# Kernel optimization log

Hardware: AMD Instinct MI355X
Metric: run time of the kernel (lower is better)

Reference implementation:

```python
import jax, jax.numpy as jnp
import numpy as np
import math

DIM = 1024
N_HEADS = 16
HEAD_DIM = DIM // N_HEADS


def rope(x):
    # x: [B, H, S, D] with D == HEAD_DIM, interleaved even/odd rotation
    S = x.shape[-2]
    D = x.shape[-1]
    pos = jnp.arange(S, dtype=x.dtype)[:, None]              # [S, 1]
    dim = jnp.arange(D // 2, dtype=x.dtype)[None, :]         # [1, D/2]
    theta = pos / jnp.exp(2.0 * dim / D * math.log(10000.0))  # [S, D/2]
    sin = jnp.sin(theta)[None, None]                          # [1,1,S,D/2]
    cos = jnp.cos(theta)[None, None]
    x1 = x[..., ::2]
    x2 = x[..., 1::2]
    out1 = x1 * cos - x2 * sin
    out2 = x1 * sin + x2 * cos
    # interleave back: stack on last axis then flatten pairs
    return jnp.stack([out1, out2], axis=-1).reshape(x.shape)


def setup_inputs() -> dict:
    key = jax.random.key(0)
    ks = jax.random.split(key, 9)
    B, S = 2, 2048
    s = 1.0 / math.sqrt(DIM)
    inp = {
        "x": jax.random.normal(ks[0], (B, S, DIM), dtype=jnp.float32),
        "wq": jax.random.normal(ks[1], (DIM, DIM), dtype=jnp.float32) * s,
        "bq": jnp.zeros((DIM,), dtype=jnp.float32),
        "wk": jax.random.normal(ks[2], (DIM, DIM), dtype=jnp.float32) * s,
        "bk": jnp.zeros((DIM,), dtype=jnp.float32),
        "wv": jax.random.normal(ks[3], (DIM, DIM), dtype=jnp.float32) * s,
        "bv": jnp.zeros((DIM,), dtype=jnp.float32),
        "wo": jax.random.normal(ks[4], (DIM, DIM), dtype=jnp.float32) * s,
        "bo": jnp.zeros((DIM,), dtype=jnp.float32),
    }
    return inp


def reference(x, wq, bq, wk, bk, wv, bv, wo, bo):
    B, S, _ = x.shape
    # torch Linear: y = x @ W^T + b
    def proj(w, b):
        y = jnp.einsum('bsd,ed->bse', x, w) + b
        return y.reshape(B, S, N_HEADS, HEAD_DIM).transpose(0, 2, 1, 3)  # [B,H,S,Dh]
    q = rope(proj(wq, bq))
    k = rope(proj(wk, bk))
    v = proj(wv, bv)
    score = jnp.einsum('bhqd,bhkd->bhqk', q, k) / math.sqrt(HEAD_DIM)
    causal = jnp.tril(jnp.ones((S, S), dtype=bool))
    score = jnp.where(causal[None, None], score, -jnp.inf)
    attn = jax.nn.softmax(score, axis=-1)
    out = jnp.einsum('bhqk,bhkd->bhqd', attn, v)
    out = out.transpose(0, 2, 1, 3).reshape(B, S, DIM)
    return jnp.einsum('bsd,ed->bse', out, wo) + bo
```

## Files before the change

### kernel.cpp

```cpp
#include <hip/hip_runtime.h>
#include <cstdint>
#include <cstddef>
#include <cmath>


typedef __bf16 bf16_t;
typedef __bf16 bf16x8 __attribute__((ext_vector_type(8)));
typedef __bf16 bf16x4 __attribute__((ext_vector_type(4)));
typedef float  f32x4  __attribute__((ext_vector_type(4)));

#define DEVFN __device__ __forceinline__

static constexpr int Bn  = 2;
static constexpr int S   = 2048;
static constexpr int DIM = 1024;
static constexpr int NH  = 16;
static constexpr int HD  = 64;
static constexpr int Mrows = Bn * S;

DEVFN f32x4 mfma16(bf16x8 a, bf16x8 b, f32x4 c) {
  return __builtin_amdgcn_mfma_f32_16x16x32_bf16(a, b, c, 0, 0, 0);
}

DEVFN void gl_lds16(const bf16_t* g, bf16_t* l) {
  __builtin_amdgcn_global_load_lds(
      (const __attribute__((address_space(1))) unsigned*)g,
      (__attribute__((address_space(3))) unsigned*)l, 16, 0, 0);
}

DEVFN float fast_exp2(float x) { return exp2f(x); }

__global__ __launch_bounds__(256) void k_prep(
    const float* __restrict__ x, const float* __restrict__ wq,
    const float* __restrict__ wk, const float* __restrict__ wv,
    const float* __restrict__ wo, bf16_t* __restrict__ xb,
    bf16_t* __restrict__ wqb, bf16_t* __restrict__ wkb,
    bf16_t* __restrict__ wvb, bf16_t* __restrict__ wob,
    float2* __restrict__ tab) {
  const int bid = blockIdx.x;
  if (bid < 8192) {
    const float* src;
    bf16_t* dst;
    size_t base;
    if (bid < 4096) {
      src = x; dst = xb; base = (size_t)bid << 10;
    } else {
      int wsel = (bid - 4096) >> 10;
      src = wsel == 0 ? wq : wsel == 1 ? wk : wsel == 2 ? wv : wo;
      dst = wsel == 0 ? wqb : wsel == 1 ? wkb : wsel == 2 ? wvb : wob;
      base = (size_t)((bid - 4096) & 1023) << 10;
    }
    size_t i = base + (size_t)threadIdx.x * 4;
    float4 v = *(const float4*)(src + i);
    bf16x4 o = { (bf16_t)v.x, (bf16_t)v.y, (bf16_t)v.z, (bf16_t)v.w };
    *(bf16x4*)(dst + i) = o;
  } else {
    int i = (bid - 8192) * 256 + threadIdx.x;
    int s = i >> 5, d = i & 31;
    float th = (float)s * expf((float)d * -0.2878231366f);
    tab[i] = make_float2(cosf(th), sinf(th));
  }
}

__global__ __launch_bounds__(256) void k_gemm_qkv(
    const bf16_t* __restrict__ A, const bf16_t* __restrict__ Wall,
    const float* __restrict__ c0, const float* __restrict__ c1,
    const float* __restrict__ c2, bf16_t* __restrict__ Oq,
    bf16_t* __restrict__ Ok, bf16_t* __restrict__ VTo,
    const float2* __restrict__ tab) {
  __shared__ __align__(16) bf16_t Al[128 * 64];
  __shared__ __align__(16) bf16_t Bl[64 * 64];
  const int t = threadIdx.x, w = t >> 6, l = t & 63;
  const int lr = l & 15, lc = l >> 4;
  const int lid = blockIdx.x;
  const int xcd = lid & 7, s = lid >> 3;
  const int my = ((xcd >> 1) << 3) + (s & 7);
  const int nx = (xcd & 1) * 24 + (s >> 3);
  const int m0 = my * 128, n0g = nx * 64;
  const int z = n0g >> 10, n0l = n0g & 1023;
  f32x4 acc[2][4] = {};

  for (int k0 = 0; k0 < DIM; k0 += 64) {
    __syncthreads();
#pragma unroll
    for (int ld = 0; ld < 4; ++ld) {
      int c = t + ld * 256;
      int row = c >> 3;
      int j = ((c & 7) ^ (row & 7)) << 3;
      gl_lds16(A + (size_t)(m0 + row) * DIM + k0 + j,
               Al + (size_t)(w * 64 + ld * 256) * 8);
    }
#pragma unroll
    for (int ld = 0; ld < 2; ++ld) {
      int c = t + ld * 256;
      int row = c >> 3;
      int j = ((c & 7) ^ (row & 7)) << 3;
      gl_lds16(Wall + (size_t)(n0g + row) * DIM + k0 + j,
               Bl + (size_t)(w * 64 + ld * 256) * 8);
    }
    asm volatile("s_waitcnt vmcnt(0)" ::: "memory");
    __syncthreads();
    bf16x8 af[2][2], bfr[2][4];
#pragma unroll
    for (int ks = 0; ks < 2; ++ks) {
#pragma unroll
      for (int mi = 0; mi < 2; ++mi) {
        int row = w * 32 + mi * 16 + lr;
        int off = ((ks * 4 + lc) << 4) ^ ((row & 7) << 4);
        af[ks][mi] = *(const bf16x8*)((const char*)Al + row * 128 + off);
      }
#pragma unroll
      for (int ni = 0; ni < 4; ++ni) {
        int row = ni * 16 + lr;
        int off = ((ks * 4 + lc) << 4) ^ ((row & 7) << 4);
        bfr[ks][ni] = *(const bf16x8*)((const char*)Bl + row * 128 + off);
      }
    }
    __builtin_amdgcn_s_setprio(1);
#pragma unroll
    for (int ks = 0; ks < 2; ++ks)
#pragma unroll
      for (int mi = 0; mi < 2; ++mi)
#pragma unroll
        for (int ni = 0; ni < 4; ++ni)
          acc[mi][ni] = mfma16(af[ks][mi], bfr[ks][ni], acc[mi][ni]);
    __builtin_amdgcn_s_setprio(0);
  }

  if (z == 2) {
    const int h = n0l >> 6;
#pragma unroll
    for (int ni = 0; ni < 4; ++ni) {
      const int d = ni * 16 + lr;
      const float bv = c2[n0l + ni * 16 + lr];
#pragma unroll
      for (int mi = 0; mi < 2; ++mi) {
        int rowb = m0 + w * 32 + mi * 16 + lc * 4;
        int bb = rowb >> 11, ss = rowb & (S - 1);
        bf16x4 pb = { (bf16_t)(acc[mi][ni][0] + bv),
                      (bf16_t)(acc[mi][ni][1] + bv),
                      (bf16_t)(acc[mi][ni][2] + bv),
                      (bf16_t)(acc[mi][ni][3] + bv) };
        *(bf16x4*)(VTo + ((size_t)(bb * NH + h) * HD + d) * S + ss) = pb;
      }
    }
  } else {
    bf16_t* Ov = z == 0 ? Oq : Ok;
    const float* bias = z == 0 ? c0 : c1;
    const float scale = z == 0 ? 0.125f * 1.4426950408889634f : 1.0f;
#pragma unroll
    for (int ni = 0; ni < 4; ++ni) {
      const int col = n0l + ni * 16 + lr;
      const float bv = bias[col];
      const int p0 = ni * 8 + (lr >> 1);
#pragma unroll
      for (int mi = 0; mi < 2; ++mi) {
#pragma unroll
        for (int r = 0; r < 4; ++r) {
          int row = m0 + w * 32 + mi * 16 + lc * 4 + r;
          float v = acc[mi][ni][r] + bv;
          float pt = __shfl_xor(v, 1);
          float2 cs = tab[(row & (S - 1)) * 32 + p0];
          float out = (lr & 1) ? (pt * cs.y + v * cs.x)
                               : (v * cs.x - pt * cs.y);
          Ov[(size_t)row * DIM + col] = (bf16_t)(out * scale);
        }
      }
    }
  }
}

__global__ __launch_bounds__(256) void k_gemm_out(
    const bf16_t* __restrict__ A, const bf16_t* __restrict__ Bw,
    const float* __restrict__ bias, float* __restrict__ Ov) {
  __shared__ __align__(16) bf16_t Al[64 * 64];
  __shared__ __align__(16) bf16_t Bl[64 * 64];
  const int t = threadIdx.x, w = t >> 6, l = t & 63;
  const int lr = l & 15, lc = l >> 4;
  const int lid = blockIdx.x;
  const int xcd = lid & 7, s = lid >> 3;
  const int my = ((xcd >> 1) << 4) + (s & 15);
  const int nx = (xcd & 1) * 8 + (s >> 4);
  const int m0 = my * 64, n0 = nx * 64;
  f32x4 acc[4] = {};

  for (int k0 = 0; k0 < DIM; k0 += 64) {
    __syncthreads();
#pragma unroll
    for (int ld = 0; ld < 2; ++ld) {
      int c = t + ld * 256;
      int row = c >> 3;
      int j = ((c & 7) ^ (row & 7)) << 3;
      gl_lds16(A + (size_t)(m0 + row) * DIM + k0 + j,
               Al + (size_t)(w * 64 + ld * 256) * 8);
    }
#pragma unroll
    for (int ld = 0; ld < 2; ++ld) {
      int c = t + ld * 256;
      int row = c >> 3;
      int j = ((c & 7) ^ (row & 7)) << 3;
      gl_lds16(Bw + (size_t)(n0 + row) * DIM + k0 + j,
               Bl + (size_t)(w * 64 + ld * 256) * 8);
    }
    asm volatile("s_waitcnt vmcnt(0)" ::: "memory");
    __syncthreads();
    bf16x8 af[2], bfr[2][4];
#pragma unroll
    for (int ks = 0; ks < 2; ++ks) {
      int arow = w * 16 + lr;
      int aoff = ((ks * 4 + lc) << 4) ^ ((arow & 7) << 4);
      af[ks] = *(const bf16x8*)((const char*)Al + arow * 128 + aoff);
#pragma unroll
      for (int ni = 0; ni < 4; ++ni) {
        int row = ni * 16 + lr;
        int off = ((ks * 4 + lc) << 4) ^ ((row & 7) << 4);
        bfr[ks][ni] = *(const bf16x8*)((const char*)Bl + row * 128 + off);
      }
    }
    __builtin_amdgcn_s_setprio(1);
#pragma unroll
    for (int ks = 0; ks < 2; ++ks)
#pragma unroll
      for (int ni = 0; ni < 4; ++ni)
        acc[ni] = mfma16(af[ks], bfr[ks][ni], acc[ni]);
    __builtin_amdgcn_s_setprio(0);
  }

#pragma unroll
  for (int ni = 0; ni < 4; ++ni) {
    int col = n0 + ni * 16 + lr;
    float bv = bias[col];
#pragma unroll
    for (int r = 0; r < 4; ++r) {
      int row = m0 + w * 16 + lc * 4 + r;
      Ov[(size_t)row * DIM + col] = acc[ni][r] + bv;
    }
  }
}

DEVFN void stage_kv(const bf16_t* __restrict__ Kc,
                    const bf16_t* __restrict__ VT, bf16_t* Kb, bf16_t* Vb,
                    int b, int bh, int h, int k0, int tid, int w) {
#pragma unroll
  for (int ld = 0; ld < 2; ++ld) {
    int c = tid + ld * 256;
    int row = c >> 3;
    int j = ((c & 7) ^ (row & 7)) << 3;
    bf16_t* dstK = Kb + (size_t)(w * 64 + ld * 256) * 8;
    bf16_t* dstV = Vb + (size_t)(w * 64 + ld * 256) * 8;
    gl_lds16(Kc + (size_t)(b * S + k0 + row) * DIM + h * HD + j, dstK);
    gl_lds16(VT + ((size_t)bh * HD + row) * S + k0 + j, dstV);
  }
}

__global__ __launch_bounds__(256) void k_attn(const bf16_t* __restrict__ Q,
                                              const bf16_t* __restrict__ Kc,
                                              const bf16_t* __restrict__ VT,
                                              bf16_t* __restrict__ O) {
  __shared__ __align__(16) bf16_t Kl[64 * 64];
  __shared__ __align__(16) bf16_t Vl[64 * 64];
  __shared__ __align__(16) bf16_t Pl[4][16 * 64];
  const int tid = threadIdx.x, w = tid >> 6, l = tid & 63;
  const int lr = l & 15, lc = l >> 4;
  const int lid = blockIdx.x;
  const int xcd = lid & 7;
  const int rest = lid >> 3;
  const int t_ord = rest >> 2;
  const int hh = rest & 3;
  const int tile = 31 - t_ord;
  const int bh = xcd * 4 + hh;
  const int b = bh >> 4, h = bh & 15;
  char* Pw = (char*)&Pl[w][0];

  const int q0 = tile * 64;
  const int nt = tile + 1;

  bf16x8 qf[2];
  {
    const bf16_t* qp =
        Q + (size_t)(b * S + q0 + w * 16 + lr) * DIM + h * HD + lc * 8;
    qf[0] = *(const bf16x8*)qp;
    qf[1] = *(const bf16x8*)(qp + 32);
  }
  f32x4 o[4] = {};
  float m_run = -INFINITY;
  float rowsum = 0.f;

#pragma unroll 1
  for (int it = 0; it < nt; ++it) {
    stage_kv(Kc, VT, &Kl[0], &Vl[0], b, bh, h, it * 64, tid, w);
    asm volatile("s_waitcnt vmcnt(0)" ::: "memory");
    __builtin_amdgcn_s_barrier();
    __builtin_amdgcn_sched_barrier(0);

    f32x4 s[4] = {};
    __builtin_amdgcn_s_setprio(1);
#pragma unroll
    for (int ks = 0; ks < 2; ++ks) {
#pragma unroll
      for (int ni = 0; ni < 4; ++ni) {
        int row = ni * 16 + lr;
        int off = (ks * 64 + lc * 16) ^ ((row & 7) << 4);
        bf16x8 kf = *(const bf16x8*)((const char*)Kl + row * 128 + off);
        s[ni] = mfma16(kf, qf[ks], s[ni]);
      }
    }
    __builtin_amdgcn_s_setprio(0);

    if (it == tile) {
      const int qloc = w * 16 + lr;
#pragma unroll
      for (int ni = 0; ni < 4; ++ni)
#pragma unroll
        for (int r = 0; r < 4; ++r)
          if (ni * 16 + lc * 4 + r > qloc) s[ni][r] = -INFINITY;
    }

    float m01 = fmaxf(fmaxf(s[0][0], s[0][1]), fmaxf(s[0][2], s[0][3]));
    float m23 = fmaxf(fmaxf(s[1][0], s[1][1]), fmaxf(s[1][2], s[1][3]));
    float m45 = fmaxf(fmaxf(s[2][0], s[2][1]), fmaxf(s[2][2], s[2][3]));
    float m67 = fmaxf(fmaxf(s[3][0], s[3][1]), fmaxf(s[3][2], s[3][3]));
    float pm = fmaxf(fmaxf(m01, m23), fmaxf(m45, m67));
    pm = fmaxf(pm, __shfl_xor(pm, 16));
    pm = fmaxf(pm, __shfl_xor(pm, 32));

    if (__ballot(pm > m_run + 8.f)) {
      float mn = fmaxf(m_run, pm);
      float alpha = fast_exp2(m_run - mn);
      m_run = mn;
      rowsum *= alpha;
#pragma unroll
      for (int r = 0; r < 4; ++r) {
        float aq = __shfl(alpha, lc * 4 + r);
#pragma unroll
        for (int ni = 0; ni < 4; ++ni) o[ni][r] *= aq;
      }
    }

    float rs = 0.f;
#pragma unroll
    for (int ni = 0; ni < 4; ++ni) {
      float p0 = fast_exp2(s[ni][0] - m_run);
      float p1 = fast_exp2(s[ni][1] - m_run);
      float p2 = fast_exp2(s[ni][2] - m_run);
      float p3 = fast_exp2(s[ni][3] - m_run);
      rs += (p0 + p1) + (p2 + p3);
      bf16x4 pb = { (bf16_t)p0, (bf16_t)p1, (bf16_t)p2, (bf16_t)p3 };
      *(bf16x4*)(Pw + (lr * 128 + ((ni * 32 + lc * 8) ^ ((lr & 7) << 4)))) =
          pb;
    }
    rs += __shfl_xor(rs, 16);
    rs += __shfl_xor(rs, 32);
    rowsum += rs;

    __builtin_amdgcn_s_setprio(1);
#pragma unroll
    for (int ks = 0; ks < 2; ++ks) {
      int off = ks * 64 + lc * 16;
      bf16x8 pa = *(const bf16x8*)(Pw + lr * 128 + (off ^ ((lr & 7) << 4)));
#pragma unroll
      for (int ni = 0; ni < 4; ++ni) {
        int vrow = ni * 16 + lr;
        bf16x8 vb = *(const bf16x8*)((const char*)Vl + vrow * 128 +
                                     (off ^ ((vrow & 7) << 4)));
        o[ni] = mfma16(pa, vb, o[ni]);
      }
    }
    __builtin_amdgcn_s_setprio(0);

    __builtin_amdgcn_s_barrier();
  }

  float inv[4];
#pragma unroll
  for (int r = 0; r < 4; ++r) inv[r] = 1.0f / __shfl(rowsum, lc * 4 + r);
#pragma unroll
  for (int ni = 0; ni < 4; ++ni)
#pragma unroll
    for (int r = 0; r < 4; ++r) {
      int qr = q0 + w * 16 + lc * 4 + r;
      float v = o[ni][r] * inv[r];
      O[(size_t)(b * S + qr) * DIM + h * HD + ni * 16 + lr] = (bf16_t)v;
    }
}

extern "C" void kernel_launch(void* const* d_in, const int* in_sizes, int n_in,
                              void* d_out, int out_size, void* d_ws,
                              size_t ws_size, hipStream_t stream) {
  const float* x  = (const float*)d_in[0];
  const float* wq = (const float*)d_in[1];
  const float* bq = (const float*)d_in[2];
  const float* wk = (const float*)d_in[3];
  const float* bk = (const float*)d_in[4];
  const float* wv = (const float*)d_in[5];
  const float* bv = (const float*)d_in[6];
  const float* wo = (const float*)d_in[7];
  const float* bo = (const float*)d_in[8];

  const size_t MD = (size_t)Mrows * DIM;
  const size_t WD = (size_t)DIM * DIM;
  bf16_t* W = (bf16_t*)d_ws;
  bf16_t* x_bf  = W;
  bf16_t* wq_bf = x_bf + MD;
  bf16_t* wk_bf = wq_bf + WD;
  bf16_t* wv_bf = wk_bf + WD;
  bf16_t* wo_bf = wv_bf + WD;
  bf16_t* q_lin = wo_bf + WD;
  bf16_t* k_lin = q_lin + MD;
  bf16_t* v_lin = k_lin + MD;
  bf16_t* vT    = v_lin + MD;
  float2* tab   = (float2*)(vT + MD);
  bf16_t* attn_out = x_bf;

  k_prep<<<8448, 256, 0, stream>>>(x, wq, wk, wv, wo, x_bf, wq_bf, wk_bf,
                                   wv_bf, wo_bf, tab);

  k_gemm_qkv<<<1536, 256, 0, stream>>>(x_bf, wq_bf, bq, bk, bv, q_lin, k_lin,
                                       vT, tab);

  k_attn<<<1024, 256, 0, stream>>>(q_lin, k_lin, vT, attn_out);

  k_gemm_out<<<1024, 256, 0, stream>>>(attn_out, wo_bf, bo, (float*)d_out);
}
```

Measured before the change: 114.5 us.

## Switch attention to 32x32x16 MFMA with two waves per 64-row query tile

Rewrites the attention kernel so each of two waves owns 32 query rows and uses the 32x32x16 bf16 MFMA instead of 16x16x32, halving the block to 128 threads. The larger MFMA tile raises operand reuse per LDS read and cuts cross-lane shuffles in the row max and sum reductions. The trade-off is fewer waves per block to hide global-to-LDS staging latency, plus more accumulator registers per thread, which may lower occupancy.

```diff
diff --git a/kernel.cpp b/kernel.cpp
--- a/kernel.cpp
+++ b/kernel.cpp
@@ -8,6 +8,7 @@
 typedef __bf16 bf16x8 __attribute__((ext_vector_type(8)));
 typedef __bf16 bf16x4 __attribute__((ext_vector_type(4)));
 typedef float  f32x4  __attribute__((ext_vector_type(4)));
+typedef float  f32x16 __attribute__((ext_vector_type(16)));
 
 #define DEVFN __device__ __forceinline__
 
@@ -20,6 +21,9 @@
 
 DEVFN f32x4 mfma16(bf16x8 a, bf16x8 b, f32x4 c) {
   return __builtin_amdgcn_mfma_f32_16x16x32_bf16(a, b, c, 0, 0, 0);
+}
+DEVFN f32x16 mfma32(bf16x8 a, bf16x8 b, f32x16 c) {
+  return __builtin_amdgcn_mfma_f32_32x32x16_bf16(a, b, c, 0, 0, 0);
 }
 
 DEVFN void gl_lds16(const bf16_t* g, bf16_t* l) {
@@ -238,30 +242,30 @@
   }
 }
 
-DEVFN void stage_kv(const bf16_t* __restrict__ Kc,
-                    const bf16_t* __restrict__ VT, bf16_t* Kb, bf16_t* Vb,
-                    int b, int bh, int h, int k0, int tid, int w) {
-#pragma unroll
-  for (int ld = 0; ld < 2; ++ld) {
-    int c = tid + ld * 256;
+DEVFN void stage_kv128(const bf16_t* __restrict__ Kc,
+                       const bf16_t* __restrict__ VT, bf16_t* Kb, bf16_t* Vb,
+                       int b, int bh, int h, int k0, int tid, int w) {
+#pragma unroll
+  for (int ld = 0; ld < 4; ++ld) {
+    int c = tid + ld * 128;
     int row = c >> 3;
     int j = ((c & 7) ^ (row & 7)) << 3;
-    bf16_t* dstK = Kb + (size_t)(w * 64 + ld * 256) * 8;
-    bf16_t* dstV = Vb + (size_t)(w * 64 + ld * 256) * 8;
+    bf16_t* dstK = Kb + (size_t)(w * 64 + ld * 128) * 8;
+    bf16_t* dstV = Vb + (size_t)(w * 64 + ld * 128) * 8;
     gl_lds16(Kc + (size_t)(b * S + k0 + row) * DIM + h * HD + j, dstK);
     gl_lds16(VT + ((size_t)bh * HD + row) * S + k0 + j, dstV);
   }
 }
 
-__global__ __launch_bounds__(256) void k_attn(const bf16_t* __restrict__ Q,
+__global__ __launch_bounds__(128) void k_attn(const bf16_t* __restrict__ Q,
                                               const bf16_t* __restrict__ Kc,
                                               const bf16_t* __restrict__ VT,
                                               bf16_t* __restrict__ O) {
   __shared__ __align__(16) bf16_t Kl[64 * 64];
   __shared__ __align__(16) bf16_t Vl[64 * 64];
-  __shared__ __align__(16) bf16_t Pl[4][16 * 64];
+  __shared__ __align__(16) bf16_t Pl[2][32 * 64];
   const int tid = threadIdx.x, w = tid >> 6, l = tid & 63;
-  const int lr = l & 15, lc = l >> 4;
+  const int l31 = l & 31, hi = l >> 5;
   const int lid = blockIdx.x;
   const int xcd = lid & 7;
   const int rest = lid >> 3;
@@ -271,57 +275,60 @@
   const int bh = xcd * 4 + hh;
   const int b = bh >> 4, h = bh & 15;
   char* Pw = (char*)&Pl[w][0];
+  const int swz = (l31 & 7) << 4;
 
   const int q0 = tile * 64;
   const int nt = tile + 1;
-
-  bf16x8 qf[2];
+  const int qg = q0 + w * 32 + l31;
+
+  bf16x8 qf[4];
   {
-    const bf16_t* qp =
-        Q + (size_t)(b * S + q0 + w * 16 + lr) * DIM + h * HD + lc * 8;
+    const bf16_t* qp = Q + (size_t)(b * S + qg) * DIM + h * HD + hi * 8;
     qf[0] = *(const bf16x8*)qp;
-    qf[1] = *(const bf16x8*)(qp + 32);
-  }
-  f32x4 o[4] = {};
+    qf[1] = *(const bf16x8*)(qp + 16);
+    qf[2] = *(const bf16x8*)(qp + 32);
+    qf[3] = *(const bf16x8*)(qp + 48);
+  }
+  f32x16 o0 = {}, o1 = {};
   float m_run = -INFINITY;
   float rowsum = 0.f;
 
 #pragma unroll 1
   for (int it = 0; it < nt; ++it) {
-    stage_kv(Kc, VT, &Kl[0], &Vl[0], b, bh, h, it * 64, tid, w);
+    stage_kv128(Kc, VT, &Kl[0], &Vl[0], b, bh, h, it * 64, tid, w);
     asm volatile("s_waitcnt vmcnt(0)" ::: "memory");
     __builtin_amdgcn_s_barrier();
     __builtin_amdgcn_sched_barrier(0);
 
-    f32x4 s[4] = {};
+    f32x16 s0 = {}, s1 = {};
     __builtin_amdgcn_s_setprio(1);
 #pragma unroll
-    for (int ks = 0; ks < 2; ++ks) {
-#pragma unroll
-      for (int ni = 0; ni < 4; ++ni) {
-        int row = ni * 16 + lr;
-        int off = (ks * 64 + lc * 16) ^ ((row & 7) << 4);
-        bf16x8 kf = *(const bf16x8*)((const char*)Kl + row * 128 + off);
-        s[ni] = mfma16(kf, qf[ks], s[ni]);
-      }
+    for (int t = 0; t < 4; ++t) {
+      int boff = t * 32 + hi * 16;
+      bf16x8 kf0 = *(const bf16x8*)((const char*)Kl + l31 * 128 +
+                                    (boff ^ swz));
+      bf16x8 kf1 = *(const bf16x8*)((const char*)Kl + (32 + l31) * 128 +
+                                    (boff ^ swz));
+      s0 = mfma32(kf0, qf[t], s0);
+      s1 = mfma32(kf1, qf[t], s1);
     }
     __builtin_amdgcn_s_setprio(0);
 
     if (it == tile) {
-      const int qloc = w * 16 + lr;
-#pragma unroll
-      for (int ni = 0; ni < 4; ++ni)
-#pragma unroll
-        for (int r = 0; r < 4; ++r)
-          if (ni * 16 + lc * 4 + r > qloc) s[ni][r] = -INFINITY;
-    }
-
-    float m01 = fmaxf(fmaxf(s[0][0], s[0][1]), fmaxf(s[0][2], s[0][3]));
-    float m23 = fmaxf(fmaxf(s[1][0], s[1][1]), fmaxf(s[1][2], s[1][3]));
-    float m45 = fmaxf(fmaxf(s[2][0], s[2][1]), fmaxf(s[2][2], s[2][3]));
-    float m67 = fmaxf(fmaxf(s[3][0], s[3][1]), fmaxf(s[3][2], s[3][3]));
-    float pm = fmaxf(fmaxf(m01, m23), fmaxf(m45, m67));
-    pm = fmaxf(pm, __shfl_xor(pm, 16));
+      const int qloc = w * 32 + l31;
+#pragma unroll
+      for (int reg = 0; reg < 16; ++reg) {
+        int kvr = (reg & 3) + 8 * (reg >> 2) + 4 * hi;
+        if (kvr > qloc) s0[reg] = -INFINITY;
+        if (32 + kvr > qloc) s1[reg] = -INFINITY;
+      }
+    }
+
+    float pm = s0[0];
+#pragma unroll
+    for (int reg = 1; reg < 16; ++reg) pm = fmaxf(pm, s0[reg]);
+#pragma unroll
+    for (int reg = 0; reg < 16; ++reg) pm = fmaxf(pm, s1[reg]);
     pm = fmaxf(pm, __shfl_xor(pm, 32));
 
     if (__ballot(pm > m_run + 8.f)) {
@@ -330,58 +337,63 @@
       m_run = mn;
       rowsum *= alpha;
 #pragma unroll
-      for (int r = 0; r < 4; ++r) {
-        float aq = __shfl(alpha, lc * 4 + r);
-#pragma unroll
-        for (int ni = 0; ni < 4; ++ni) o[ni][r] *= aq;
+      for (int reg = 0; reg < 16; ++reg) {
+        int qrow = (reg & 3) + 8 * (reg >> 2) + 4 * hi;
+        float aq = __shfl(alpha, qrow);
+        o0[reg] *= aq;
+        o1[reg] *= aq;
       }
     }
 
     float rs = 0.f;
 #pragma unroll
-    for (int ni = 0; ni < 4; ++ni) {
-      float p0 = fast_exp2(s[ni][0] - m_run);
-      float p1 = fast_exp2(s[ni][1] - m_run);
-      float p2 = fast_exp2(s[ni][2] - m_run);
-      float p3 = fast_exp2(s[ni][3] - m_run);
-      rs += (p0 + p1) + (p2 + p3);
-      bf16x4 pb = { (bf16_t)p0, (bf16_t)p1, (bf16_t)p2, (bf16_t)p3 };
-      *(bf16x4*)(Pw + (lr * 128 + ((ni * 32 + lc * 8) ^ ((lr & 7) << 4)))) =
-          pb;
-    }
-    rs += __shfl_xor(rs, 16);
+    for (int g = 0; g < 4; ++g) {
+      float a0 = fast_exp2(s0[4 * g + 0] - m_run);
+      float a1 = fast_exp2(s0[4 * g + 1] - m_run);
+      float a2 = fast_exp2(s0[4 * g + 2] - m_run);
+      float a3 = fast_exp2(s0[4 * g + 3] - m_run);
+      rs += (a0 + a1) + (a2 + a3);
+      bf16x4 pb = { (bf16_t)a0, (bf16_t)a1, (bf16_t)a2, (bf16_t)a3 };
+      *(bf16x4*)(Pw + l31 * 128 + ((g * 16 + hi * 8) ^ swz)) = pb;
+      float b0 = fast_exp2(s1[4 * g + 0] - m_run);
+      float b1 = fast_exp2(s1[4 * g + 1] - m_run);
+      float b2 = fast_exp2(s1[4 * g + 2] - m_run);
+      float b3 = fast_exp2(s1[4 * g + 3] - m_run);
+      rs += (b0 + b1) + (b2 + b3);
+      bf16x4 qb = { (bf16_t)b0, (bf16_t)b1, (bf16_t)b2, (bf16_t)b3 };
+      *(bf16x4*)(Pw + l31 * 128 + ((64 + g * 16 + hi * 8) ^ swz)) = qb;
+    }
     rs += __shfl_xor(rs, 32);
     rowsum += rs;
 
     __builtin_amdgcn_s_setprio(1);
 #pragma unroll
-    for (int ks = 0; ks < 2; ++ks) {
-      int off = ks * 64 + lc * 16;
-      bf16x8 pa = *(const bf16x8*)(Pw + lr * 128 + (off ^ ((lr & 7) << 4)));
-#pragma unroll
-      for (int ni = 0; ni < 4; ++ni) {
-        int vrow = ni * 16 + lr;
-        bf16x8 vb = *(const bf16x8*)((const char*)Vl + vrow * 128 +
-                                     (off ^ ((vrow & 7) << 4)));
-        o[ni] = mfma16(pa, vb, o[ni]);
-      }
-    }
+    for (int ns = 0; ns < 2; ++ns)
+#pragma unroll
+      for (int t = 0; t < 2; ++t) {
+        int pboff = ns * 64 + t * 32 + hi * 16;
+        bf16x8 pa = *(const bf16x8*)(Pw + l31 * 128 + (pboff ^ swz));
+        bf16x8 v0 = *(const bf16x8*)((const char*)Vl + l31 * 128 +
+                                     (pboff ^ swz));
+        bf16x8 v1 = *(const bf16x8*)((const char*)Vl + (32 + l31) * 128 +
+                                     (pboff ^ swz));
+        o0 = mfma32(pa, v0, o0);
+        o1 = mfma32(pa, v1, o1);
+      }
     __builtin_amdgcn_s_setprio(0);
 
     __builtin_amdgcn_s_barrier();
   }
 
-  float inv[4];
-#pragma unroll
-  for (int r = 0; r < 4; ++r) inv[r] = 1.0f / __shfl(rowsum, lc * 4 + r);
-#pragma unroll
-  for (int ni = 0; ni < 4; ++ni)
-#pragma unroll
-    for (int r = 0; r < 4; ++r) {
-      int qr = q0 + w * 16 + lc * 4 + r;
-      float v = o[ni][r] * inv[r];
-      O[(size_t)(b * S + qr) * DIM + h * HD + ni * 16 + lr] = (bf16_t)v;
-    }
+#pragma unroll
+  for (int reg = 0; reg < 16; ++reg) {
+    int qrow = (reg & 3) + 8 * (reg >> 2) + 4 * hi;
+    float inv = 1.0f / __shfl(rowsum, qrow);
+    int qr = q0 + w * 32 + qrow;
+    bf16_t* op = O + (size_t)(b * S + qr) * DIM + h * HD + l31;
+    op[0]  = (bf16_t)(o0[reg] * inv);
+    op[32] = (bf16_t)(o1[reg] * inv);
+  }
 }
 
 extern "C" void kernel_launch(void* const* d_in, const int* in_sizes, int n_in,
@@ -418,7 +430,7 @@
   k_gemm_qkv<<<1536, 256, 0, stream>>>(x_bf, wq_bf, bq, bk, bv, q_lin, k_lin,
                                        vT, tab);
 
-  k_attn<<<1024, 256, 0, stream>>>(q_lin, k_lin, vT, attn_out);
+  k_attn<<<1024, 128, 0, stream>>>(q_lin, k_lin, vT, attn_out);
 
   k_gemm_out<<<1024, 256, 0, stream>>>(attn_out, wo_bf, bo, (float*)d_out);
 }
```

Result: slower. 126.1 us (+10.2%).
